# Performance work log

Hardware: AMD Instinct MI355X
Metric: run time of the kernel (lower is better)

## Reference

```python
import jax, jax.numpy as jnp
import numpy as np

K = 3            # kernel_size
H = 2048
W = 2048
N = 1_000_000    # number of query points
LATENT = 4
POS = 6
CTRL = 2
HID = 64
OUT = 4
IN_CH = (LATENT + POS + CTRL) * K * K  # 108


def _linear_params(key, fan_in, fan_out):
    bound = 1.0 / np.sqrt(fan_in)
    kw, kb = jax.random.split(key)
    Wm = jax.random.uniform(kw, (fan_in, fan_out), minval=-bound, maxval=bound, dtype=jnp.float32)
    bm = jax.random.uniform(kb, (fan_out,), minval=-bound, maxval=bound, dtype=jnp.float32)
    return Wm, bm


def setup_inputs() -> dict:
    key = jax.random.key(0)
    ks = jax.random.split(key, 7)
    W1, b1 = _linear_params(ks[0], IN_CH, HID)
    W2, b2 = _linear_params(ks[1], HID, 2 * HID)
    W3, b3 = _linear_params(ks[2], 2 * HID, HID)
    W4, b4 = _linear_params(ks[3], HID, OUT)
    latent = jax.random.normal(ks[4], (H, W, LATENT), dtype=jnp.float32)
    raw_pos = jax.random.randint(ks[5], (N, 2), 0, W).astype(jnp.int32)  # (x, y) coords
    control = jax.random.normal(ks[6], (N, CTRL), dtype=jnp.float32)
    return {"latent": latent, "raw_pos": raw_pos, "control": control,
            "W1": W1, "b1": b1, "W2": W2, "b2": b2,
            "W3": W3, "b3": b3, "W4": W4, "b4": b4}


def reference(latent, raw_pos, control, W1, b1, W2, b2, W3, b3, W4, b4):
    Hh, Ww, C = latent.shape
    n = raw_pos.shape[0]
    r = K // 2
    d = jnp.arange(-r, r + 1, dtype=raw_pos.dtype)
    ox, oy = jnp.meshgrid(d, d, indexing="xy")
    offsets = jnp.stack([ox.ravel(), oy.ravel()], axis=-1)          # [K*K, 2] (dx, dy)
    exp = raw_pos[:, None, :] + offsets[None, :, :]                 # [N, K*K, 2]
    ex = jnp.clip(exp[..., 0], 0, Ww - 1)
    ey = jnp.clip(exp[..., 1], 0, Hh - 1)
    lin = ey * Ww + ex                                              # linear gather indices
    latent_values = latent.reshape(-1, C)[lin]                      # [N, K*K, C] irregular gather

    xs = jnp.clip(raw_pos[:, 0:1], 0, Ww - 1).astype(latent.dtype) / Ww
    ys = jnp.clip(raw_pos[:, 1:2], 0, Hh - 1).astype(latent.dtype) / Hh
    tp = jnp.asarray(2.0 * np.pi, latent.dtype)
    # sinusoidal encoding with input included: [x, y, sin(2pi x), cos(2pi x), sin(2pi y), cos(2pi y)] -> pos_channels=6
    pos = jnp.concatenate([xs, ys, jnp.sin(tp * xs), jnp.cos(tp * xs), jnp.sin(tp * ys), jnp.cos(tp * ys)], axis=-1)
    pos_e = jnp.broadcast_to(pos[:, None, :], (n, K * K, POS))
    ctl_e = jnp.broadcast_to(control[:, None, :], (n, K * K, control.shape[-1]))

    patches = jnp.concatenate([latent_values, pos_e, ctl_e], axis=-1)  # [N, K*K, 12]
    x = patches.reshape(n, -1)                                          # [N, 108]

    h = jax.nn.gelu(x @ W1 + b1, approximate=False)
    h = jax.nn.gelu(h @ W2 + b2, approximate=False)
    h = jax.nn.gelu(h @ W3 + b3, approximate=False)
    return jax.nn.sigmoid(h @ W4 + b4)                                  # [N, 4]
```

## Files before the change

kernel.cpp:

```cpp
#include <hip/hip_runtime.h>
#include <hip/hip_fp16.h>

typedef __attribute__((ext_vector_type(8))) _Float16 half8;
typedef __attribute__((ext_vector_type(4))) float f32x4;
typedef __attribute__((ext_vector_type(4))) unsigned int uint4v;

#define HGT 2048
#define WID 2048
#define NPTS 1000000
#define NBLK 1954
#define WBYTES 44096
#define BIAS_OFF 43008

__device__ __host__ inline int c64map(int k){
  return 16*(k>>5) + 32*((k&7)>>2) + 4*((k>>3)&3) + (k&3);
}
__device__ __host__ inline int c128map(int k){
  return 16*(k>>5) + 64*((k&7)>>2) + 4*((k>>3)&3) + (k&3);
}

__global__ void prepack_kernel(const float* __restrict__ W1, const float* __restrict__ b1,
                               const float* __restrict__ W2, const float* __restrict__ b2,
                               const float* __restrict__ W3, const float* __restrict__ b3,
                               const float* __restrict__ W4, const float* __restrict__ b4,
                               unsigned short* __restrict__ packed){
  int tid = blockIdx.x*256 + threadIdx.x;
  if (tid < 42*64) {
    int f = tid >> 6, l = tid & 63;
    int fr = l & 15, kg = l >> 4;
    int layer, mt, kk;
    if (f < 8)       { layer=1; mt=f>>1;      kk=f&1; }
    else if (f < 24) { layer=2; mt=(f-8)>>1;  kk=(f-8)&1; }
    else if (f < 40) { layer=3; mt=(f-24)>>2; kk=(f-24)&3; }
    else             { layer=4; mt=0;         kk=f-40; }
    unsigned short v16[8];
    #pragma unroll
    for (int e=0;e<8;e++){
      int k = kk*32 + kg*8 + e;
      int fout = mt*16 + fr;
      float v = 0.0f;
      if (layer==1) {
        if (k < 36)      { v = W1[((k>>2)*12 + (k&3))*64 + fout]; }
        else if (k < 42) { float s=0.f; for (int p=0;p<9;p++) s += W1[(p*12+4+(k-36))*64 + fout]; v=s; }
        else if (k < 44) { float s=0.f; for (int p=0;p<9;p++) s += W1[(p*12+10+(k-42))*64 + fout]; v=s; }
      } else if (layer==2) { v = W2[c64map(k)*128 + fout]; }
      else if (layer==3)   { v = W3[c128map(k)*64 + fout]; }
      else                 { v = (fr < 4) ? W4[c64map(k)*4 + fr] : 0.0f; }
      v16[e] = __half_as_ushort(__float2half(v));
    }
    unsigned short* dst = packed + (size_t)f*512 + (size_t)l*8;
    #pragma unroll
    for (int e=0;e<8;e++) dst[e] = v16[e];
  }
  int bt = tid - 42*64;
  if (bt >= 0 && bt < 272) {
    float v;
    if (bt < 64)       v = b1[bt];
    else if (bt < 192) v = b2[bt-64];
    else if (bt < 256) v = b3[bt-192];
    else               v = (bt-256 < 4) ? b4[bt-256] : 0.0f;
    ((float*)((char*)packed + BIAS_OFF))[bt] = v;
  }
}

__device__ inline unsigned pkf(float a, float b){
  return __builtin_bit_cast(unsigned, __builtin_amdgcn_cvt_pkrtz(a, b));
}
__device__ inline float gelu1(float x){
  const float x2 = x*x;
  const float z  = x * __builtin_fmaf(0.10294913f, x2, 2.3021164f);
  const float t  = __builtin_amdgcn_exp2f(z);
  const float r  = __builtin_amdgcn_rcpf(t + 1.0f);
  return __builtin_fmaf(-x, r, x);
}
__device__ inline unsigned gelu2_v(float a, float b){
  return pkf(gelu1(a), gelu1(b));
}
__device__ inline float fast_sigmoid(float x){
  return __builtin_amdgcn_rcpf(1.0f + __builtin_amdgcn_exp2f(-1.442695041f*x));
}

template<int MT,int KT,int DKT,int FB,int BO,int J,int KIN>
__device__ __forceinline__ void layerJ(const half8* __restrict__ Wfrag, const float* __restrict__ bias,
                                       const uint4v (&in)[J][KIN], uint4v (&outp)[J][DKT],
                                       int lane, int g){
  #pragma unroll
  for (int mt=0; mt<MT; mt++){
    const f32x4 bv = *(const f32x4*)(bias + BO + mt*16 + g*4);
    f32x4 acc[J];
    #pragma unroll
    for (int j=0;j<J;j++) acc[j] = bv;
    #pragma unroll
    for (int kk=0; kk<KT; kk++){
      const half8 w = Wfrag[(FB + mt*KT + kk)*64 + lane];
      #pragma unroll
      for (int j=0;j<J;j++)
        acc[j] = __builtin_amdgcn_mfma_f32_16x16x32_f16(w, __builtin_bit_cast(half8, in[j][kk]), acc[j], 0,0,0);
    }
    #pragma unroll
    for (int j=0;j<J;j++){
      outp[j][mt%DKT][(mt/DKT)*2+0] = gelu2_v(acc[j][0], acc[j][1]);
      outp[j][mt%DKT][(mt/DKT)*2+1] = gelu2_v(acc[j][2], acc[j][3]);
    }
  }
}

__global__ __launch_bounds__(1024, 8)
void decoder_kernel(const float* __restrict__ latent, const int* __restrict__ raw_pos,
                    const float* __restrict__ control, const unsigned short* __restrict__ packed,
                    float* __restrict__ out){
  __shared__ __attribute__((aligned(16))) char smem[WBYTES];
  const int tid = threadIdx.x;
  const int wave = tid >> 6, lane = tid & 63;
  const int nlo = lane & 15, g = lane >> 4;
  const int pA = g*2, pB = g*2+1;
  const int qA = (pA>=3) + (pA>=6), qB = (pB>=3) + (pB>=6);
  const int dyA = qA-1, dxA = pA-3*qA-1;
  const int dyB = qB-1, dxB = pB-3*qB-1;

  const int R0 = blockIdx.x*512 + wave*32;

  int2 xyv[2];
  #pragma unroll
  for (int jj=0; jj<2; jj++){
    const int prow = min(R0 + jj*16 + nlo, NPTS-1);
    xyv[jj] = ((const int2*)raw_pos)[prow];
  }

  {
    const f32x4* src = (const f32x4*)packed;
    f32x4* dst = (f32x4*)smem;
    for (int i = tid; i < WBYTES/16; i += 1024) dst[i] = src[i];
  }

  uint4v bx[2][2];
  #pragma unroll
  for (int jj=0; jj<2; jj++){
    const int2 xy = xyv[jj];
    const int exA = min(max(xy.x + dxA, 0), WID-1);
    const int eyA = min(max(xy.y + dyA, 0), HGT-1);
    const int exB = min(max(xy.x + dxB, 0), WID-1);
    const int eyB = min(max(xy.y + dyB, 0), HGT-1);
    const f32x4 lA = *(const f32x4*)(latent + ((size_t)eyA*WID + exA)*4);
    const f32x4 lB = *(const f32x4*)(latent + ((size_t)eyB*WID + exB)*4);
    uint4v f0;
    f0.x = pkf(lA[0], lA[1]); f0.y = pkf(lA[2], lA[3]);
    f0.z = pkf(lB[0], lB[1]); f0.w = pkf(lB[2], lB[3]);

    const float xs = (float)xy.x * (1.0f/WID), ys = (float)xy.y * (1.0f/HGT);
    const float sx = __builtin_amdgcn_sinf(xs), cx = __builtin_amdgcn_cosf(xs);
    const float sy = __builtin_amdgcn_sinf(ys), cy = __builtin_amdgcn_cosf(ys);
    uint4v f1; f1.x = 0u; f1.y = 0u; f1.z = 0u; f1.w = 0u;
    if (g == 0){
      const int ex8 = min(xy.x + 1, WID-1), ey8 = min(xy.y + 1, HGT-1);
      const f32x4 l8 = *(const f32x4*)(latent + ((size_t)ey8*WID + ex8)*4);
      f1.x = pkf(l8[0], l8[1]); f1.y = pkf(l8[2], l8[3]);
      f1.z = pkf(xs, ys); f1.w = pkf(sx, cx);
    } else if (g == 1){
      const int prow = min(R0 + jj*16 + nlo, NPTS-1);
      const float2 ct = ((const float2*)control)[prow];
      f1.x = pkf(sy, cy); f1.y = pkf(ct.x, ct.y);
    }
    bx[jj][0] = f0; bx[jj][1] = f1;
  }
  __syncthreads();

  const half8* Wfrag = (const half8*)smem;
  const float* bias  = (const float*)(smem + BIAS_OFF);

  uint4v h1[2][2], h2[2][4], h3[2][2];
  layerJ<4,2,2, 0,  0,2,2>(Wfrag, bias, bx, h1, lane, g);
  layerJ<8,2,4, 8, 64,2,2>(Wfrag, bias, h1, h2, lane, g);
  layerJ<4,4,2,24,192,2,4>(Wfrag, bias, h2, h3, lane, g);

  const f32x4 bv4 = *(const f32x4*)(bias + 256 + g*4);
  f32x4 a = bv4, b = bv4;
  #pragma unroll
  for (int kk=0; kk<2; kk++){
    const half8 w = Wfrag[(40+kk)*64 + lane];
    a = __builtin_amdgcn_mfma_f32_16x16x32_f16(w, __builtin_bit_cast(half8, h3[0][kk]), a, 0,0,0);
    b = __builtin_amdgcn_mfma_f32_16x16x32_f16(w, __builtin_bit_cast(half8, h3[1][kk]), b, 0,0,0);
  }
  if (g == 0){
    f32x4 oa, ob;
    #pragma unroll
    for (int j=0;j<4;j++){ oa[j] = fast_sigmoid(a[j]); ob[j] = fast_sigmoid(b[j]); }
    if (R0 < NPTS)      *(f32x4*)(out + (size_t)(R0 + nlo)*4)      = oa;
    if (R0 + 16 < NPTS) *(f32x4*)(out + (size_t)(R0 + 16 + nlo)*4) = ob;
  }
}

extern "C" void kernel_launch(void* const* d_in, const int* in_sizes, int n_in,
                              void* d_out, int out_size, void* d_ws, size_t ws_size,
                              hipStream_t stream) {
  const float* latent  = (const float*)d_in[0];
  const int*   raw_pos = (const int*)d_in[1];
  const float* control = (const float*)d_in[2];
  const float* W1 = (const float*)d_in[3];
  const float* b1 = (const float*)d_in[4];
  const float* W2 = (const float*)d_in[5];
  const float* b2 = (const float*)d_in[6];
  const float* W3 = (const float*)d_in[7];
  const float* b3 = (const float*)d_in[8];
  const float* W4 = (const float*)d_in[9];
  const float* b4 = (const float*)d_in[10];
  unsigned short* packed = (unsigned short*)d_ws;

  prepack_kernel<<<12, 256, 0, stream>>>(W1,b1,W2,b2,W3,b3,W4,b4,packed);
  decoder_kernel<<<NBLK, 1024, 0, stream>>>(latent, raw_pos, control, packed, (float*)d_out);
}
```

Before: 133.5 us.

## Use rational GELU approximation, smaller 512-thread blocks, and reorder weight staging

Replaces the exp-based GELU approximation with a clamped rational polynomial in packed float2 form, which needs one reciprocal and no exp per element. Blocks shrink from 1024 to 512 threads with twice as many blocks and different launch bounds, which changes occupancy and the per-block cost of copying weights. Weight staging into shared memory now happens before the gathers, so it no longer overlaps the latent loads. The rational fit is only approximate and its accuracy near the clamp edges may differ from the old form.

```diff
diff --git a/kernel.cpp b/kernel.cpp
--- a/kernel.cpp
+++ b/kernel.cpp
@@ -3,12 +3,13 @@
 
 typedef __attribute__((ext_vector_type(8))) _Float16 half8;
 typedef __attribute__((ext_vector_type(4))) float f32x4;
+typedef __attribute__((ext_vector_type(2))) float f32x2;
 typedef __attribute__((ext_vector_type(4))) unsigned int uint4v;
 
 #define HGT 2048
 #define WID 2048
 #define NPTS 1000000
-#define NBLK 1954
+#define NTILES 3907
 #define WBYTES 44096
 #define BIAS_OFF 43008
 
@@ -66,15 +67,20 @@
 __device__ inline unsigned pkf(float a, float b){
   return __builtin_bit_cast(unsigned, __builtin_amdgcn_cvt_pkrtz(a, b));
 }
-__device__ inline float gelu1(float x){
-  const float x2 = x*x;
-  const float z  = x * __builtin_fmaf(0.10294913f, x2, 2.3021164f);
-  const float t  = __builtin_amdgcn_exp2f(z);
-  const float r  = __builtin_amdgcn_rcpf(t + 1.0f);
-  return __builtin_fmaf(-x, r, x);
-}
 __device__ inline unsigned gelu2_v(float a, float b){
-  return pkf(gelu1(a), gelu1(b));
+  f32x2 x  = {a, b};
+  f32x2 xc = { __builtin_amdgcn_fmed3f(a, -4.0f, 4.0f),
+               __builtin_amdgcn_fmed3f(b, -4.0f, 4.0f) };
+  f32x2 s  = xc * xc;
+  f32x2 num = __builtin_elementwise_fma(s, (f32x2){0.0026758f,0.0026758f}, (f32x2){0.0986155f,0.0986155f});
+  num = __builtin_elementwise_fma(num, s, (f32x2){0.3989423f,0.3989423f});
+  f32x2 den = __builtin_elementwise_fma(s, (f32x2){0.0535340f,0.0535340f}, (f32x2){0.4119460f,0.4119460f});
+  den = __builtin_elementwise_fma(den, s, (f32x2){1.0f,1.0f});
+  f32x2 rd = { __builtin_amdgcn_rcpf(den.x), __builtin_amdgcn_rcpf(den.y) };
+  f32x2 m  = (x * xc) * rd;
+  f32x2 hx = x * (f32x2){0.5f,0.5f};
+  f32x2 gl = __builtin_elementwise_fma(m, num, hx);
+  return pkf(gl.x, gl.y);
 }
 __device__ inline float fast_sigmoid(float x){
   return __builtin_amdgcn_rcpf(1.0f + __builtin_amdgcn_exp2f(-1.442695041f*x));
@@ -105,12 +111,21 @@
   }
 }
 
-__global__ __launch_bounds__(1024, 8)
+__global__ __launch_bounds__(512, 6)
 void decoder_kernel(const float* __restrict__ latent, const int* __restrict__ raw_pos,
                     const float* __restrict__ control, const unsigned short* __restrict__ packed,
                     float* __restrict__ out){
   __shared__ __attribute__((aligned(16))) char smem[WBYTES];
   const int tid = threadIdx.x;
+  {
+    const f32x4* src = (const f32x4*)packed;
+    f32x4* dst = (f32x4*)smem;
+    for (int i = tid; i < WBYTES/16; i += 512) dst[i] = src[i];
+  }
+  __syncthreads();
+
+  const half8* Wfrag = (const half8*)smem;
+  const float* bias  = (const float*)(smem + BIAS_OFF);
   const int wave = tid >> 6, lane = tid & 63;
   const int nlo = lane & 15, g = lane >> 4;
   const int pA = g*2, pB = g*2+1;
@@ -118,25 +133,13 @@
   const int dyA = qA-1, dxA = pA-3*qA-1;
   const int dyB = qB-1, dxB = pB-3*qB-1;
 
-  const int R0 = blockIdx.x*512 + wave*32;
-
-  int2 xyv[2];
+  const int R0 = blockIdx.x*256 + wave*32;
+
+  uint4v bx[2][2];
   #pragma unroll
   for (int jj=0; jj<2; jj++){
     const int prow = min(R0 + jj*16 + nlo, NPTS-1);
-    xyv[jj] = ((const int2*)raw_pos)[prow];
-  }
-
-  {
-    const f32x4* src = (const f32x4*)packed;
-    f32x4* dst = (f32x4*)smem;
-    for (int i = tid; i < WBYTES/16; i += 1024) dst[i] = src[i];
-  }
-
-  uint4v bx[2][2];
-  #pragma unroll
-  for (int jj=0; jj<2; jj++){
-    const int2 xy = xyv[jj];
+    const int2 xy = ((const int2*)raw_pos)[prow];
     const int exA = min(max(xy.x + dxA, 0), WID-1);
     const int eyA = min(max(xy.y + dyA, 0), HGT-1);
     const int exB = min(max(xy.x + dxB, 0), WID-1);
@@ -157,16 +160,11 @@
       f1.x = pkf(l8[0], l8[1]); f1.y = pkf(l8[2], l8[3]);
       f1.z = pkf(xs, ys); f1.w = pkf(sx, cx);
     } else if (g == 1){
-      const int prow = min(R0 + jj*16 + nlo, NPTS-1);
       const float2 ct = ((const float2*)control)[prow];
       f1.x = pkf(sy, cy); f1.y = pkf(ct.x, ct.y);
     }
     bx[jj][0] = f0; bx[jj][1] = f1;
   }
-  __syncthreads();
-
-  const half8* Wfrag = (const half8*)smem;
-  const float* bias  = (const float*)(smem + BIAS_OFF);
 
   uint4v h1[2][2], h2[2][4], h3[2][2];
   layerJ<4,2,2, 0,  0,2,2>(Wfrag, bias, bx, h1, lane, g);
@@ -207,5 +205,5 @@
   unsigned short* packed = (unsigned short*)d_ws;
 
   prepack_kernel<<<12, 256, 0, stream>>>(W1,b1,W2,b2,W3,b3,W4,b4,packed);
-  decoder_kernel<<<NBLK, 1024, 0, stream>>>(latent, raw_pos, control, packed, (float*)d_out);
-}
+  decoder_kernel<<<NTILES, 512, 0, stream>>>(latent, raw_pos, control, packed, (float*)d_out);
+}
```

Measured after the change: 119.6 us. 10.4% less time.
